# Performance work log

Hardware: AMD Instinct MI355X
Metric: run time of the kernel (lower is better)

Reference implementation:

```python
import jax, jax.numpy as jnp
import numpy as np

B, S, D, H = 2, 2048, 1024, 16
DK = D // H


def setup_inputs() -> dict:
    key = jax.random.key(0)
    ks = jax.random.split(key, 14)
    inp = {
        'query': jax.random.normal(ks[0], (B, S, D), jnp.float32),
        'key': jax.random.normal(ks[1], (B, S, D), jnp.float32),
        'value': jax.random.normal(ks[2], (B, S, D), jnp.float32),
        'mask': jax.random.randint(ks[3], (B, 1, S, S), 0, 2).astype(bool),
        'rel_pos_bias': jax.random.normal(ks[4], (1, H, S, S), jnp.float32),
    }
    scale = 1.0 / np.sqrt(D)
    names = ['Wq', 'bq', 'Wk', 'bk', 'Wv', 'bv', 'Wo', 'bo']
    for i, n in enumerate(names):
        k = ks[5 + i]
        if n.startswith('W'):
            inp[n] = jax.random.normal(k, (D, D), jnp.float32) * scale
        else:
            inp[n] = jnp.zeros((D,), jnp.float32)
    return inp


def reference(query, key, value, mask, rel_pos_bias, Wq, bq, Wk, bk, Wv, bv, Wo, bo):
    # torch Linear: y = x @ W^T + b; W stored [out, in]
    def proj(x, W, b):
        y = x @ W.T + b                       # [B,S,D]
        return y.reshape(B, S, H, DK).transpose(0, 2, 1, 3)  # [B,H,S,DK]

    q = proj(query, Wq, bq)
    k = proj(key, Wk, bk)
    v = proj(value, Wv, bv)

    scores = jnp.einsum('bhqd,bhkd->bhqk', q, k) / jnp.sqrt(jnp.float32(DK))
    scores = scores + rel_pos_bias
    scores = jnp.where(mask, jnp.float32(-1e9), scores)
    p_attn = jax.nn.softmax(scores, axis=-1)
    x = jnp.einsum('bhqk,bhkd->bhqd', p_attn, v)  # [B,H,S,DK]
    x = x.transpose(0, 2, 1, 3).reshape(B, S, D)
    return x @ Wo.T + bo
```

## Files before the change

### kernel.cpp

```cpp
#include <hip/hip_runtime.h>
#include <stdint.h>


typedef _Float16 f16;
typedef _Float16 f16x8 __attribute__((ext_vector_type(8)));
typedef _Float16 f16x4 __attribute__((ext_vector_type(4)));
typedef float f32x4 __attribute__((ext_vector_type(4)));

#define LOG2E 1.44269504088896340736f

__device__ __forceinline__ void gload16(const void* g, void* l) {
  __builtin_amdgcn_global_load_lds(
      (const __attribute__((address_space(1))) unsigned int*)g,
      (__attribute__((address_space(3))) unsigned int*)l, 16, 0, 0);
}

__global__ __launch_bounds__(256) void cvt_f32_f16(const float* __restrict__ in,
                                                   f16* __restrict__ out, int n4) {
  const int i = blockIdx.x * 256 + threadIdx.x;
  if (i >= n4) return;
  const float4 v = ((const float4*)in)[i];
  f16x4 o = {(f16)v.x, (f16)v.y, (f16)v.z, (f16)v.w};
  ((f16x4*)out)[i] = o;
}

__global__ void mask_detect(const uint8_t* __restrict__ m, int* __restrict__ flag) {
  __shared__ int s_off, s_weird;
  const int t = threadIdx.x;
  if (t == 0) { s_off = 0; s_weird = 0; }
  __syncthreads();
  int f_off = 0, f_weird = 0;
  for (int i = t; i < 8192; i += 256) {
    const uint8_t v = m[i];
    if ((i & 3) && v) f_off = 1;
    if (v > 1) f_weird = 1;
  }
  if (f_off) atomicOr(&s_off, 1);
  if (f_weird) atomicOr(&s_weird, 1);
  __syncthreads();
  if (t == 0) *flag = (s_off && !s_weird) ? 1 : 0;
}

__global__ __launch_bounds__(256) void mask_canon(const uint8_t* __restrict__ m,
                                                  uint8_t* __restrict__ out,
                                                  const int* __restrict__ flag) {
  const int i = (blockIdx.x * 256 + threadIdx.x) * 4;
  uchar4 o;
  if (*flag) {
    const uchar4 v = *(const uchar4*)(m + i);
    o = make_uchar4(v.x != 0, v.y != 0, v.z != 0, v.w != 0);
  } else {
    const int4 v = *(const int4*)((const int*)m + i);
    o = make_uchar4(v.x != 0, v.y != 0, v.z != 0, v.w != 0);
  }
  *(uchar4*)(out + i) = o;
}

template <int MODE>
__global__ __launch_bounds__(256, 2) void gemm_bt(const f16* __restrict__ A,
                                                  const f16* __restrict__ Bw,
                                                  const float* __restrict__ bias,
                                                  void* __restrict__ outp) {
  constexpr int K = 1024;
  const int t = threadIdx.x;
  const int w = t >> 6, lane = t & 63, l15 = lane & 15, l4 = lane >> 4;
  const int bm = (int)(blockIdx.x >> 4) * 128;
  const int bn = (int)(blockIdx.x & 15) * 64;

  __shared__ f16 As[2][128 * 32];
  __shared__ f16 Bs[2][64 * 32];

  const f16* a0 = A + (size_t)(bm + (t >> 2)) * K + (t & 3) * 8;
  const f16* a1 = a0 + (size_t)64 * K;
  const f16* b0 = Bw + (size_t)(bn + (t >> 2)) * K + (t & 3) * 8;

  f32x4 acc[2][4];
#pragma unroll
  for (int m = 0; m < 2; ++m)
#pragma unroll
    for (int n = 0; n < 4; ++n) acc[m][n] = (f32x4){0.f, 0.f, 0.f, 0.f};

#define STAGE_G(buf, k0)                          \
  do {                                            \
    gload16(a0 + (k0), &As[buf][w * 512]);        \
    gload16(a1 + (k0), &As[buf][2048 + w * 512]); \
    gload16(b0 + (k0), &Bs[buf][w * 512]);        \
  } while (0)

  STAGE_G(0, 0);
  __syncthreads();
  int cur = 0;
#pragma unroll 1
  for (int kt = 0; kt < 32; ++kt) {
    if (kt < 31) STAGE_G(cur ^ 1, (kt + 1) * 32);
    const f16* ap = &As[cur][(w * 32 + l15) * 32 + l4 * 8];
    const f16* bp = &Bs[cur][l15 * 32 + l4 * 8];
    f16x8 af[2], bfr[4];
#pragma unroll
    for (int m = 0; m < 2; ++m) af[m] = *(const f16x8*)(ap + m * 512);
#pragma unroll
    for (int n = 0; n < 4; ++n) bfr[n] = *(const f16x8*)(bp + n * 512);
#pragma unroll
    for (int m = 0; m < 2; ++m)
#pragma unroll
      for (int n = 0; n < 4; ++n)
        acc[m][n] = __builtin_amdgcn_mfma_f32_16x16x32_f16(af[m], bfr[n], acc[m][n], 0, 0, 0);
    __syncthreads();
    cur ^= 1;
  }
#undef STAGE_G

#pragma unroll
  for (int m = 0; m < 2; ++m) {
    const int r0 = bm + w * 32 + m * 16 + (l4 << 2);
#pragma unroll
    for (int n = 0; n < 4; ++n) {
      const int c = bn + n * 16 + l15;
      const float bv = bias[c];
#pragma unroll
      for (int j = 0; j < 4; ++j) {
        const int r = r0 + j;
        const float v = acc[m][n][j] + bv;
        if (MODE == 0) {
          const int b_ = r >> 11, s = r & 2047, h_ = c >> 6, dk = c & 63;
          ((f16*)outp)[(((size_t)b_ * 16 + h_) * 2048 + s) * 64 + dk] = (f16)v;
        } else if (MODE == 1) {
          const int b_ = r >> 11, s = r & 2047, h_ = c >> 6, dk = c & 63;
          ((f16*)outp)[(((size_t)b_ * 16 + h_) * 64 + dk) * 2048 + s] = (f16)v;
        } else {
          ((float*)outp)[(size_t)r * 1024 + c] = v;
        }
      }
    }
  }
}

__device__ __forceinline__ const f16x8* swzr(const f16* base, int row, int bytecol) {
  return (const f16x8*)((const char*)base + row * 128 + (bytecol ^ ((row & 7) << 4)));
}

__global__ __launch_bounds__(256, 2) void attn_fwd(
    const f16* __restrict__ Qp, const f16* __restrict__ Kp,
    const f16* __restrict__ Vt, const float* __restrict__ bias,
    const uint8_t* __restrict__ mask, f16* __restrict__ X) {
  constexpr int S = 2048;
  const int bid = blockIdx.x;
  const int qt = bid & 15, b = (bid >> 4) & 1, h = bid >> 5;
  const int t = threadIdx.x, w = t >> 6, lane = t & 63;
  const int l15 = lane & 15, l4 = lane >> 4;
  const int q0 = qt * 128 + w * 32;

  const f16* Qbh = Qp + (size_t)(b * 16 + h) * S * 64;
  const f16* Kbh = Kp + (size_t)(b * 16 + h) * S * 64;
  const f16* Vbh = Vt + (size_t)(b * 16 + h) * 64 * S;
  const float* biash = bias + (size_t)h * S * S;
  const uint8_t* maskb = mask + (size_t)b * S * S;

  __shared__ f16 Ks[64 * 64];
  __shared__ f16 Vs[64 * 64];
  __shared__ f16 Ps[4][32 * 64];

  f16x8 qf[2][2];
#pragma unroll
  for (int m = 0; m < 2; ++m)
#pragma unroll
    for (int ks = 0; ks < 2; ++ks)
      qf[m][ks] = *(const f16x8*)(Qbh + (size_t)(q0 + m * 16 + l15) * 64 + ks * 32 + l4 * 8);

  f32x4 oacc[2][4];
#pragma unroll
  for (int m = 0; m < 2; ++m)
#pragma unroll
    for (int n = 0; n < 4; ++n) oacc[m][n] = (f32x4){0.f, 0.f, 0.f, 0.f};
  float mrow[2][4], lrow[2][4];
#pragma unroll
  for (int m = 0; m < 2; ++m)
#pragma unroll
    for (int j = 0; j < 4; ++j) { mrow[m][j] = -3e38f; lrow[m][j] = 0.f; }

  const int srow = t >> 3;
  const int scol = (((t & 7) ^ (srow & 7)) << 3);

#pragma unroll 1
  for (int kt = 0; kt < 32; ++kt) {
    const int k0 = kt * 64;
    __syncthreads();
    gload16(Kbh + (size_t)(k0 + srow) * 64 + scol, &Ks[w * 512]);
    gload16(Kbh + (size_t)(k0 + 32 + srow) * 64 + scol, &Ks[2048 + w * 512]);
    gload16(Vbh + (size_t)srow * S + k0 + scol, &Vs[w * 512]);
    gload16(Vbh + (size_t)(32 + srow) * S + k0 + scol, &Vs[2048 + w * 512]);
    __syncthreads();

    f32x4 sacc[2][4];
#pragma unroll
    for (int m = 0; m < 2; ++m)
#pragma unroll
      for (int n = 0; n < 4; ++n) sacc[m][n] = (f32x4){0.f, 0.f, 0.f, 0.f};
    f16x8 kf[4][2];
#pragma unroll
    for (int n = 0; n < 4; ++n)
#pragma unroll
      for (int ks = 0; ks < 2; ++ks)
        kf[n][ks] = *swzr(Ks, n * 16 + l15, ks * 64 + l4 * 16);
#pragma unroll
    for (int m = 0; m < 2; ++m)
#pragma unroll
      for (int n = 0; n < 4; ++n)
#pragma unroll
        for (int ks = 0; ks < 2; ++ks)
          sacc[m][n] = __builtin_amdgcn_mfma_f32_16x16x32_f16(qf[m][ks], kf[n][ks], sacc[m][n], 0, 0, 0);

    float p[2][4][4];
    float tmax[2][4];
#pragma unroll
    for (int m = 0; m < 2; ++m)
#pragma unroll
      for (int j = 0; j < 4; ++j) tmax[m][j] = -3e38f;
#pragma unroll
    for (int m = 0; m < 2; ++m) {
#pragma unroll
      for (int j = 0; j < 4; ++j) {
        const int qrow = q0 + m * 16 + l4 * 4 + j;
        const float* brow = biash + (size_t)qrow * S + k0;
        const uint8_t* mrw = maskb + (size_t)qrow * S + k0;
#pragma unroll
        for (int n = 0; n < 4; ++n) {
          const int kc = n * 16 + l15;
          float s = sacc[m][n][j] * 0.125f + brow[kc];
          s = mrw[kc] ? -1e9f : s;
          p[m][n][j] = s;
          tmax[m][j] = fmaxf(tmax[m][j], s);
        }
      }
    }
#pragma unroll
    for (int m = 0; m < 2; ++m)
#pragma unroll
      for (int j = 0; j < 4; ++j) {
        float v = tmax[m][j];
        v = fmaxf(v, __shfl_xor(v, 1));
        v = fmaxf(v, __shfl_xor(v, 2));
        v = fmaxf(v, __shfl_xor(v, 4));
        v = fmaxf(v, __shfl_xor(v, 8));
        tmax[m][j] = v;
      }

#pragma unroll
    for (int m = 0; m < 2; ++m) {
#pragma unroll
      for (int j = 0; j < 4; ++j) {
        const float mnew = fmaxf(mrow[m][j], tmax[m][j]);
        const float alpha = __builtin_exp2f((mrow[m][j] - mnew) * LOG2E);
        mrow[m][j] = mnew;
        lrow[m][j] *= alpha;
#pragma unroll
        for (int n = 0; n < 4; ++n) oacc[m][n][j] *= alpha;
        float lsum = 0.f;
        const int prow = m * 16 + l4 * 4 + j;
#pragma unroll
        for (int n = 0; n < 4; ++n) {
          const float e = __builtin_exp2f((p[m][n][j] - mnew) * LOG2E);
          lsum += e;
          const int bc = (n * 16 + l15) * 2;
          *(f16*)((char*)&Ps[w][0] + prow * 128 + (bc ^ ((prow & 7) << 4))) = (f16)e;
        }
        lsum += __shfl_xor(lsum, 1);
        lsum += __shfl_xor(lsum, 2);
        lsum += __shfl_xor(lsum, 4);
        lsum += __shfl_xor(lsum, 8);
        lrow[m][j] += lsum;
      }
    }

    f16x8 pf[2][2];
#pragma unroll
    for (int m = 0; m < 2; ++m)
#pragma unroll
      for (int ks = 0; ks < 2; ++ks)
        pf[m][ks] = *swzr(&Ps[w][0], m * 16 + l15, ks * 64 + l4 * 16);
#pragma unroll
    for (int ks = 0; ks < 2; ++ks)
#pragma unroll
      for (int n = 0; n < 4; ++n) {
        const f16x8 vf = *swzr(Vs, n * 16 + l15, ks * 64 + l4 * 16);
#pragma unroll
        for (int m = 0; m < 2; ++m)
          oacc[m][n] = __builtin_amdgcn_mfma_f32_16x16x32_f16(pf[m][ks], vf, oacc[m][n], 0, 0, 0);
      }
  }

#pragma unroll
  for (int m = 0; m < 2; ++m) {
#pragma unroll
    for (int j = 0; j < 4; ++j) {
      const float inv = 1.0f / lrow[m][j];
      const int qrow = q0 + m * 16 + l4 * 4 + j;
#pragma unroll
      for (int n = 0; n < 4; ++n) {
        const int dk = n * 16 + l15;
        X[((size_t)b * 2048 + qrow) * 1024 + h * 64 + dk] = (f16)(oacc[m][n][j] * inv);
      }
    }
  }
}

extern "C" void kernel_launch(void* const* d_in, const int* in_sizes, int n_in,
                              void* d_out, int out_size, void* d_ws, size_t ws_size,
                              hipStream_t stream) {
  const float* query = (const float*)d_in[0];
  const float* key_ = (const float*)d_in[1];
  const float* value = (const float*)d_in[2];
  const uint8_t* mask = (const uint8_t*)d_in[3];
  const float* bias = (const float*)d_in[4];
  const float* Wq = (const float*)d_in[5];
  const float* bq = (const float*)d_in[6];
  const float* Wk = (const float*)d_in[7];
  const float* bk = (const float*)d_in[8];
  const float* Wv = (const float*)d_in[9];
  const float* bv = (const float*)d_in[10];
  const float* Wo = (const float*)d_in[11];
  const float* bo = (const float*)d_in[12];

  char* p = (char*)d_ws;
  f16* qh = (f16*)p; p += (size_t)4194304 * 2;
  f16* kh = (f16*)p; p += (size_t)4194304 * 2;
  f16* vh = (f16*)p; p += (size_t)4194304 * 2;
  f16* wqh = (f16*)p; p += (size_t)1048576 * 2;
  f16* wkh = (f16*)p; p += (size_t)1048576 * 2;
  f16* wvh = (f16*)p; p += (size_t)1048576 * 2;
  f16* woh = (f16*)p; p += (size_t)1048576 * 2;
  f16* Qp = (f16*)p; p += (size_t)4194304 * 2;
  f16* Kp = (f16*)p; p += (size_t)4194304 * 2;
  f16* Vt = (f16*)p; p += (size_t)4194304 * 2;
  f16* Xh = (f16*)p; p += (size_t)4194304 * 2;
  uint8_t* m8 = (uint8_t*)p; p += (size_t)8388608;
  int* flag = (int*)p; p += 256;
  if (ws_size < (size_t)(p - (char*)d_ws)) return;

  mask_detect<<<1, 256, 0, stream>>>(mask, flag);
  mask_canon<<<8192, 256, 0, stream>>>(mask, m8, flag);

  cvt_f32_f16<<<4096, 256, 0, stream>>>(query, qh, 1048576);
  cvt_f32_f16<<<4096, 256, 0, stream>>>(key_, kh, 1048576);
  cvt_f32_f16<<<4096, 256, 0, stream>>>(value, vh, 1048576);
  cvt_f32_f16<<<1024, 256, 0, stream>>>(Wq, wqh, 262144);
  cvt_f32_f16<<<1024, 256, 0, stream>>>(Wk, wkh, 262144);
  cvt_f32_f16<<<1024, 256, 0, stream>>>(Wv, wvh, 262144);
  cvt_f32_f16<<<1024, 256, 0, stream>>>(Wo, woh, 262144);

  gemm_bt<0><<<512, 256, 0, stream>>>(qh, wqh, bq, Qp);
  gemm_bt<0><<<512, 256, 0, stream>>>(kh, wkh, bk, Kp);
  gemm_bt<1><<<512, 256, 0, stream>>>(vh, wvh, bv, Vt);

  attn_fwd<<<512, 256, 0, stream>>>(Qp, Kp, Vt, bias, m8, Xh);

  gemm_bt<2><<<512, 256, 0, stream>>>(Xh, woh, bo, d_out);
}
```

Before: 295.8 us.

## Halve attention query tile per wave, double grid, prefetch bias/mask before barrier

Each wave of the attention kernel now handles 16 query rows instead of 32, so the grid doubles to 1024 blocks and launch bounds ask for 4 blocks per CU. This gives more parallelism and occupancy on a 256-CU device where 512 blocks underfill it. The bias and mask loads for the tile are issued before the barrier into registers, so their latency overlaps the K/V staging. In exchange, each K/V tile is loaded into LDS by twice as many blocks, doubling K/V traffic per query row.

```diff
diff --git a/kernel.cpp b/kernel.cpp
--- a/kernel.cpp
+++ b/kernel.cpp
@@ -139,16 +139,16 @@
   return (const f16x8*)((const char*)base + row * 128 + (bytecol ^ ((row & 7) << 4)));
 }
 
-__global__ __launch_bounds__(256, 2) void attn_fwd(
+__global__ __launch_bounds__(256, 4) void attn_fwd(
     const f16* __restrict__ Qp, const f16* __restrict__ Kp,
     const f16* __restrict__ Vt, const float* __restrict__ bias,
     const uint8_t* __restrict__ mask, f16* __restrict__ X) {
   constexpr int S = 2048;
   const int bid = blockIdx.x;
-  const int qt = bid & 15, b = (bid >> 4) & 1, h = bid >> 5;
+  const int qt = bid & 31, b = (bid >> 5) & 1, h = bid >> 6;
   const int t = threadIdx.x, w = t >> 6, lane = t & 63;
   const int l15 = lane & 15, l4 = lane >> 4;
-  const int q0 = qt * 128 + w * 32;
+  const int q0 = qt * 64 + w * 16;
 
   const f16* Qbh = Qp + (size_t)(b * 16 + h) * S * 64;
   const f16* Kbh = Kp + (size_t)(b * 16 + h) * S * 64;
@@ -158,25 +158,23 @@
 
   __shared__ f16 Ks[64 * 64];
   __shared__ f16 Vs[64 * 64];
-  __shared__ f16 Ps[4][32 * 64];
-
-  f16x8 qf[2][2];
-#pragma unroll
-  for (int m = 0; m < 2; ++m)
-#pragma unroll
-    for (int ks = 0; ks < 2; ++ks)
-      qf[m][ks] = *(const f16x8*)(Qbh + (size_t)(q0 + m * 16 + l15) * 64 + ks * 32 + l4 * 8);
-
-  f32x4 oacc[2][4];
-#pragma unroll
-  for (int m = 0; m < 2; ++m)
-#pragma unroll
-    for (int n = 0; n < 4; ++n) oacc[m][n] = (f32x4){0.f, 0.f, 0.f, 0.f};
-  float mrow[2][4], lrow[2][4];
-#pragma unroll
-  for (int m = 0; m < 2; ++m)
-#pragma unroll
-    for (int j = 0; j < 4; ++j) { mrow[m][j] = -3e38f; lrow[m][j] = 0.f; }
+  __shared__ f16 Ps[4][16 * 64];
+
+  int ro[4];
+#pragma unroll
+  for (int j = 0; j < 4; ++j) ro[j] = (q0 + l4 * 4 + j) * S + l15;
+
+  f16x8 qf[2];
+#pragma unroll
+  for (int ks = 0; ks < 2; ++ks)
+    qf[ks] = *(const f16x8*)(Qbh + (size_t)(q0 + l15) * 64 + ks * 32 + l4 * 8);
+
+  f32x4 oacc[4];
+#pragma unroll
+  for (int n = 0; n < 4; ++n) oacc[n] = (f32x4){0.f, 0.f, 0.f, 0.f};
+  float mrow[4], lrow[4];
+#pragma unroll
+  for (int j = 0; j < 4; ++j) { mrow[j] = -3e38f; lrow[j] = 0.f; }
 
   const int srow = t >> 3;
   const int scol = (((t & 7) ^ (srow & 7)) << 3);
@@ -189,117 +187,96 @@
     gload16(Kbh + (size_t)(k0 + 32 + srow) * 64 + scol, &Ks[2048 + w * 512]);
     gload16(Vbh + (size_t)srow * S + k0 + scol, &Vs[w * 512]);
     gload16(Vbh + (size_t)(32 + srow) * S + k0 + scol, &Vs[2048 + w * 512]);
+    float breg[4][4];
+    int mreg[4][4];
+#pragma unroll
+    for (int j = 0; j < 4; ++j)
+#pragma unroll
+      for (int n = 0; n < 4; ++n) {
+        breg[j][n] = biash[ro[j] + k0 + n * 16];
+        mreg[j][n] = maskb[ro[j] + k0 + n * 16];
+      }
     __syncthreads();
 
-    f32x4 sacc[2][4];
-#pragma unroll
-    for (int m = 0; m < 2; ++m)
-#pragma unroll
-      for (int n = 0; n < 4; ++n) sacc[m][n] = (f32x4){0.f, 0.f, 0.f, 0.f};
-    f16x8 kf[4][2];
+    f32x4 sacc[4];
+#pragma unroll
+    for (int n = 0; n < 4; ++n) sacc[n] = (f32x4){0.f, 0.f, 0.f, 0.f};
 #pragma unroll
     for (int n = 0; n < 4; ++n)
 #pragma unroll
-      for (int ks = 0; ks < 2; ++ks)
-        kf[n][ks] = *swzr(Ks, n * 16 + l15, ks * 64 + l4 * 16);
-#pragma unroll
-    for (int m = 0; m < 2; ++m)
-#pragma unroll
-      for (int n = 0; n < 4; ++n)
-#pragma unroll
-        for (int ks = 0; ks < 2; ++ks)
-          sacc[m][n] = __builtin_amdgcn_mfma_f32_16x16x32_f16(qf[m][ks], kf[n][ks], sacc[m][n], 0, 0, 0);
-
-    float p[2][4][4];
-    float tmax[2][4];
-#pragma unroll
-    for (int m = 0; m < 2; ++m)
-#pragma unroll
-      for (int j = 0; j < 4; ++j) tmax[m][j] = -3e38f;
-#pragma unroll
-    for (int m = 0; m < 2; ++m) {
-#pragma unroll
-      for (int j = 0; j < 4; ++j) {
-        const int qrow = q0 + m * 16 + l4 * 4 + j;
-        const float* brow = biash + (size_t)qrow * S + k0;
-        const uint8_t* mrw = maskb + (size_t)qrow * S + k0;
-#pragma unroll
-        for (int n = 0; n < 4; ++n) {
-          const int kc = n * 16 + l15;
-          float s = sacc[m][n][j] * 0.125f + brow[kc];
-          s = mrw[kc] ? -1e9f : s;
-          p[m][n][j] = s;
-          tmax[m][j] = fmaxf(tmax[m][j], s);
-        }
-      }
+      for (int ks = 0; ks < 2; ++ks) {
+        const f16x8 kf = *swzr(Ks, n * 16 + l15, ks * 64 + l4 * 16);
+        sacc[n] = __builtin_amdgcn_mfma_f32_16x16x32_f16(qf[ks], kf, sacc[n], 0, 0, 0);
+      }
+
+    float p[4][4];
+    float tmax[4];
+#pragma unroll
+    for (int j = 0; j < 4; ++j) tmax[j] = -3e38f;
+#pragma unroll
+    for (int j = 0; j < 4; ++j)
+#pragma unroll
+      for (int n = 0; n < 4; ++n) {
+        float s = sacc[n][j] * 0.125f + breg[j][n];
+        s = mreg[j][n] ? -1e9f : s;
+        p[j][n] = s;
+        tmax[j] = fmaxf(tmax[j], s);
+      }
+#pragma unroll
+    for (int j = 0; j < 4; ++j) {
+      float v = tmax[j];
+      v = fmaxf(v, __shfl_xor(v, 1));
+      v = fmaxf(v, __shfl_xor(v, 2));
+      v = fmaxf(v, __shfl_xor(v, 4));
+      v = fmaxf(v, __shfl_xor(v, 8));
+      tmax[j] = v;
     }
-#pragma unroll
-    for (int m = 0; m < 2; ++m)
-#pragma unroll
-      for (int j = 0; j < 4; ++j) {
-        float v = tmax[m][j];
-        v = fmaxf(v, __shfl_xor(v, 1));
-        v = fmaxf(v, __shfl_xor(v, 2));
-        v = fmaxf(v, __shfl_xor(v, 4));
-        v = fmaxf(v, __shfl_xor(v, 8));
-        tmax[m][j] = v;
-      }
-
-#pragma unroll
-    for (int m = 0; m < 2; ++m) {
-#pragma unroll
-      for (int j = 0; j < 4; ++j) {
-        const float mnew = fmaxf(mrow[m][j], tmax[m][j]);
-        const float alpha = __builtin_exp2f((mrow[m][j] - mnew) * LOG2E);
-        mrow[m][j] = mnew;
-        lrow[m][j] *= alpha;
-#pragma unroll
-        for (int n = 0; n < 4; ++n) oacc[m][n][j] *= alpha;
-        float lsum = 0.f;
-        const int prow = m * 16 + l4 * 4 + j;
-#pragma unroll
-        for (int n = 0; n < 4; ++n) {
-          const float e = __builtin_exp2f((p[m][n][j] - mnew) * LOG2E);
-          lsum += e;
-          const int bc = (n * 16 + l15) * 2;
-          *(f16*)((char*)&Ps[w][0] + prow * 128 + (bc ^ ((prow & 7) << 4))) = (f16)e;
-        }
-        lsum += __shfl_xor(lsum, 1);
-        lsum += __shfl_xor(lsum, 2);
-        lsum += __shfl_xor(lsum, 4);
-        lsum += __shfl_xor(lsum, 8);
-        lrow[m][j] += lsum;
-      }
+
+#pragma unroll
+    for (int j = 0; j < 4; ++j) {
+      const float mnew = fmaxf(mrow[j], tmax[j]);
+      const float alpha = __builtin_exp2f((mrow[j] - mnew) * LOG2E);
+      mrow[j] = mnew;
+      lrow[j] *= alpha;
+#pragma unroll
+      for (int n = 0; n < 4; ++n) oacc[n][j] *= alpha;
+      float lsum = 0.f;
+      const int prow = l4 * 4 + j;
+#pragma unroll
+      for (int n = 0; n < 4; ++n) {
+        const float e = __builtin_exp2f((p[j][n] - mnew) * LOG2E);
+        lsum += e;
+        const int bc = (n * 16 + l15) * 2;
+        *(f16*)((char*)&Ps[w][0] + prow * 128 + (bc ^ ((prow & 7) << 4))) = (f16)e;
+      }
+      lsum += __shfl_xor(lsum, 1);
+      lsum += __shfl_xor(lsum, 2);
+      lsum += __shfl_xor(lsum, 4);
+      lsum += __shfl_xor(lsum, 8);
+      lrow[j] += lsum;
     }
 
-    f16x8 pf[2][2];
-#pragma unroll
-    for (int m = 0; m < 2; ++m)
-#pragma unroll
-      for (int ks = 0; ks < 2; ++ks)
-        pf[m][ks] = *swzr(&Ps[w][0], m * 16 + l15, ks * 64 + l4 * 16);
+    f16x8 pf[2];
+#pragma unroll
+    for (int ks = 0; ks < 2; ++ks)
+      pf[ks] = *swzr(&Ps[w][0], l15, ks * 64 + l4 * 16);
 #pragma unroll
     for (int ks = 0; ks < 2; ++ks)
 #pragma unroll
       for (int n = 0; n < 4; ++n) {
         const f16x8 vf = *swzr(Vs, n * 16 + l15, ks * 64 + l4 * 16);
-#pragma unroll
-        for (int m = 0; m < 2; ++m)
-          oacc[m][n] = __builtin_amdgcn_mfma_f32_16x16x32_f16(pf[m][ks], vf, oacc[m][n], 0, 0, 0);
-      }
-  }
-
-#pragma unroll
-  for (int m = 0; m < 2; ++m) {
-#pragma unroll
-    for (int j = 0; j < 4; ++j) {
-      const float inv = 1.0f / lrow[m][j];
-      const int qrow = q0 + m * 16 + l4 * 4 + j;
-#pragma unroll
-      for (int n = 0; n < 4; ++n) {
-        const int dk = n * 16 + l15;
-        X[((size_t)b * 2048 + qrow) * 1024 + h * 64 + dk] = (f16)(oacc[m][n][j] * inv);
-      }
+        oacc[n] = __builtin_amdgcn_mfma_f32_16x16x32_f16(pf[ks], vf, oacc[n], 0, 0, 0);
+      }
+  }
+
+#pragma unroll
+  for (int j = 0; j < 4; ++j) {
+    const float inv = 1.0f / lrow[j];
+    const int qrow = q0 + l4 * 4 + j;
+#pragma unroll
+    for (int n = 0; n < 4; ++n) {
+      const int dk = n * 16 + l15;
+      X[((size_t)b * 2048 + qrow) * 1024 + h * 64 + dk] = (f16)(oacc[n][j] * inv);
     }
   }
 }
@@ -352,7 +329,7 @@
   gemm_bt<0><<<512, 256, 0, stream>>>(kh, wkh, bk, Kp);
   gemm_bt<1><<<512, 256, 0, stream>>>(vh, wvh, bv, Vt);
 
-  attn_fwd<<<512, 256, 0, stream>>>(Qp, Kp, Vt, bias, m8, Xh);
+  attn_fwd<<<1024, 256, 0, stream>>>(Qp, Kp, Vt, bias, m8, Xh);
 
   gemm_bt<2><<<512, 256, 0, stream>>>(Xh, woh, bo, d_out);
 }
```

After: 299.6 us. No clear change (+1.3%).
